# Optimization experiments

Hardware: AMD Instinct MI355X
Metric: run time of the kernel (lower is better)

The kernel has to match this reference:

```python
import jax, jax.numpy as jnp
import numpy as np

EMBED = 1024
HEADS = 16
HEAD_DIM = EMBED // HEADS
B, S = 4, 2048


def setup_inputs() -> dict:
    key = jax.random.key(0)
    ks = jax.random.split(key, 8)
    values = jax.random.normal(ks[0], (B, S, EMBED), dtype=jnp.float32)
    keys_in = jax.random.normal(ks[1], (B, S, EMBED), dtype=jnp.float32)
    query = jax.random.normal(ks[2], (B, S, EMBED), dtype=jnp.float32)
    mask = jnp.ones((B, 1, 1, S), dtype=jnp.int32)
    sc = 1.0 / np.sqrt(HEAD_DIM)
    Wv = jax.random.normal(ks[3], (HEAD_DIM, HEAD_DIM), dtype=jnp.float32) * sc
    Wk = jax.random.normal(ks[4], (HEAD_DIM, HEAD_DIM), dtype=jnp.float32) * sc
    Wq = jax.random.normal(ks[5], (HEAD_DIM, HEAD_DIM), dtype=jnp.float32) * sc
    Wo = jax.random.normal(ks[6], (EMBED, EMBED), dtype=jnp.float32) * (1.0 / np.sqrt(EMBED))
    bo = jnp.zeros((EMBED,), dtype=jnp.float32)
    return {"values": values, "keys": keys_in, "query": query, "mask": mask,
            "Wv": Wv, "Wk": Wk, "Wq": Wq, "Wo": Wo, "bo": bo}


def reference(values, keys, query, mask, Wv, Wk, Wq, Wo, bo):
    n = query.shape[0]
    vl, kl, ql = values.shape[1], keys.shape[1], query.shape[1]
    h, d = HEADS, HEAD_DIM
    # split heads: [n, len, h, d]
    v = values.reshape(n, vl, h, d)
    k = keys.reshape(n, kl, h, d)
    q = query.reshape(n, ql, h, d)
    # per-head linear projections (torch Linear: x @ W.T), shared across heads
    v = jnp.einsum('nlhd,ed->nlhe', v, Wv)
    k = jnp.einsum('nlhd,ed->nlhe', k, Wk)
    q = jnp.einsum('nlhd,ed->nlhe', q, Wq)
    # attention scores [n, h, q, k]
    energy = jnp.einsum('nqhd,nkhd->nhqk', q, k)
    energy = jnp.where(mask == 0, jnp.float32(-1e20), energy)
    # NOTE: original scales by sqrt(embed_size), not sqrt(head_dim)
    attn = jax.nn.softmax(energy / jnp.sqrt(jnp.float32(EMBED)), axis=3)
    out = jnp.einsum('nhql,nlhd->nqhd', attn, v).reshape(n, ql, h * d)
    return out @ Wo.T + bo
```

## Files before the change

### kernel.cpp

```cpp
#include <hip/hip_runtime.h>
#include <hip/hip_bf16.h>


#define SS 2048
#define HH 16
#define DD 64

typedef __attribute__((ext_vector_type(8))) short bf16x8;
typedef __attribute__((ext_vector_type(4))) short s16x4;
typedef __attribute__((ext_vector_type(4))) float f32x4;
typedef __attribute__((ext_vector_type(16))) float f32x16;

__device__ __forceinline__ short f2bf(float f) {
  union { float f; unsigned u; } c; c.f = f;
  unsigned r = (c.u + 0x7FFFu + ((c.u >> 16) & 1u)) >> 16;
  return (short)r;
}

__device__ __forceinline__ int cvtpk(float lo, float hi) {
  int r;
  asm("v_cvt_pk_bf16_f32 %0, %1, %2" : "=v"(r) : "v"(lo), "v"(hi));
  return r;
}

__device__ __forceinline__ float fexp2(float x) {
  float r;
  asm("v_exp_f32 %0, %1" : "=v"(r) : "v"(x));
  return r;
}

__global__ __launch_bounds__(256) void proj_kernel(
    const float* __restrict__ xq, const float* __restrict__ xk, const float* __restrict__ xv,
    const float* __restrict__ Wq, const float* __restrict__ Wk, const float* __restrict__ Wv,
    short* __restrict__ qp, short* __restrict__ kp, short* __restrict__ vp)
{
  __shared__ short xlds[128][72];
  __shared__ short wlds[3][64][72];
  const int t = threadIdx.x;
  const int lane = t & 63;
  const int w = t >> 6;
  const int l15 = lane & 15, l4 = lane >> 4;

  const float* wsrc[3] = {Wq, Wk, Wv};
#pragma unroll
  for (int z = 0; z < 3; ++z) {
#pragma unroll
    for (int i = 0; i < 4; ++i) {
      int fi = (t + i * 256) * 4;
      int row = fi >> 6, col = fi & 63;
      float4 a = *(const float4*)(wsrc[z] + fi);
      s16x4 sv = { f2bf(a.x), f2bf(a.y), f2bf(a.z), f2bf(a.w) };
      *(s16x4*)&wlds[z][row][col] = sv;
    }
  }

  const long r0 = (long)blockIdx.x * 128;
  const float* xin[3] = {xq, xk, xv};
  short* outp[3] = {qp, kp, vp};
  const float SCQ = 0.03125f * 1.4426950408889634f;

#pragma unroll
  for (int z = 0; z < 3; ++z) {
    __syncthreads();
    const float* src = xin[z] + r0 * 64;
#pragma unroll
    for (int i = 0; i < 8; ++i) {
      int fi = (t + i * 256) * 4;
      int row = fi >> 6, col = fi & 63;
      float4 a = *(const float4*)(src + fi);
      s16x4 sv = { f2bf(a.x), f2bf(a.y), f2bf(a.z), f2bf(a.w) };
      *(s16x4*)&xlds[row][col] = sv;
    }
    __syncthreads();

    bf16x8 af[2][2];
#pragma unroll
    for (int mi = 0; mi < 2; ++mi)
#pragma unroll
      for (int kb = 0; kb < 2; ++kb)
        af[mi][kb] = *(const bf16x8*)&xlds[w * 32 + mi * 16 + l15][kb * 32 + l4 * 8];

    f32x4 acc[2][4];
#pragma unroll
    for (int mi = 0; mi < 2; ++mi)
#pragma unroll
      for (int nt = 0; nt < 4; ++nt)
        acc[mi][nt] = (f32x4){0.f, 0.f, 0.f, 0.f};

#pragma unroll
    for (int nt = 0; nt < 4; ++nt)
#pragma unroll
      for (int kb = 0; kb < 2; ++kb) {
        bf16x8 bfr = *(const bf16x8*)&wlds[z][nt * 16 + l15][kb * 32 + l4 * 8];
#pragma unroll
        for (int mi = 0; mi < 2; ++mi)
          acc[mi][nt] = __builtin_amdgcn_mfma_f32_16x16x32_bf16(af[mi][kb], bfr, acc[mi][nt], 0, 0, 0);
      }

    short* dst = outp[z];
    const float sc = (z == 0) ? SCQ : 1.0f;
#pragma unroll
    for (int mi = 0; mi < 2; ++mi)
#pragma unroll
      for (int nt = 0; nt < 4; ++nt)
#pragma unroll
        for (int j = 0; j < 4; ++j) {
          int r = (int)r0 + w * 32 + mi * 16 + l4 * 4 + j;
          int e = nt * 16 + l15;
          int h = r & 15, bs = r >> 4;
          int b = bs >> 11, s = bs & 2047;
          dst[(((long)(b * 16 + h) * 2048 + s) << 6) + e] = f2bf(acc[mi][nt][j] * sc);
        }
  }
}

__global__ __launch_bounds__(256) void wo_cvt(const float* __restrict__ Wo,
                                              short* __restrict__ wob) {
  long i = ((long)blockIdx.x * 256 + threadIdx.x) * 4;
  float4 a = *(const float4*)(Wo + i);
  s16x4 sv = { f2bf(a.x), f2bf(a.y), f2bf(a.z), f2bf(a.w) };
  *(s16x4*)(wob + i) = sv;
}

__global__ __launch_bounds__(256) void vt_kernel(const short* __restrict__ vp,
                                                 short* __restrict__ vpt) {
  __shared__ short tl[64][72];
  const int t = threadIdx.x;
  const long base_in = (long)blockIdx.y * SS * DD + (long)blockIdx.x * 64 * DD;
#pragma unroll
  for (int i = 0; i < 2; ++i) {
    int c = t + i * 256;
    int s = c >> 3, d0 = (c & 7) * 8;
    bf16x8 v = *(const bf16x8*)(vp + base_in + s * 64 + d0);
#pragma unroll
    for (int j = 0; j < 8; ++j) tl[d0 + j][s] = v[j];
  }
  __syncthreads();
  const long base_out = (long)blockIdx.y * DD * SS + (long)blockIdx.x * 64;
#pragma unroll
  for (int i = 0; i < 2; ++i) {
    int c = t + i * 256;
    int d = c >> 3, s0 = (c & 7) * 8;
    *(bf16x8*)(vpt + base_out + (long)d * SS + s0) = *(const bf16x8*)&tl[d][s0];
  }
}

__global__ __launch_bounds__(256, 4) void attn_kernel(
    const short* __restrict__ qp, const short* __restrict__ kp, const short* __restrict__ vpt,
    const int* __restrict__ mask, short* __restrict__ ao)
{
  __shared__ short klds[2][64][72];
  __shared__ short vtlds[2][64][72];
  __shared__ int tile_ok[32];
  const int t = threadIdx.x, lane = t & 63, w = t >> 6;
  const int l31 = lane & 31, hi = lane >> 5;
  const int wg = (blockIdx.x & 7) * 128 + (blockIdx.x >> 3);
  const int bh = wg >> 4, qt = wg & 15;
  const int b = bh >> 4, h = bh & 15;
  const short* qb  = qp + (long)bh * SS * DD;
  const short* kbp = kp + (long)bh * SS * DD;
  const short* vtp = vpt + (long)bh * DD * SS;
  const int* mb = mask + b * SS;

  if (t < 32) tile_ok[t] = 1;
  __syncthreads();
  {
    int ok = 1;
#pragma unroll
    for (int i = 0; i < 8; ++i) ok &= (mb[t * 8 + i] != 0);
    if (!ok) tile_ok[t >> 3] = 0;
  }

  const int q = qt * 128 + w * 32 + l31;
  bf16x8 qf[4];
#pragma unroll
  for (int dblk = 0; dblk < 4; ++dblk)
    qf[dblk] = *(const bf16x8*)(qb + (long)q * 64 + dblk * 16 + hi * 8);

  const int sr = t >> 2;
  const int sc = (t & 3) * 16;
  const int v5 = sr & 31;
  const int prow = (sr & 32) + (v5 & 3) + 4 * ((v5 >> 3) & 1)
                 + 8 * (2 * ((v5 >> 4) & 1) + ((v5 >> 2) & 1));
  const short* kr_ptr = kbp + (long)sr * 64 + sc;
  const short* vr_ptr = vtp + (long)sr * SS + sc;

  bf16x8 kr0 = *(const bf16x8*)(kr_ptr);
  bf16x8 kr1 = *(const bf16x8*)(kr_ptr + 8);
  bf16x8 vr0 = *(const bf16x8*)(vr_ptr);
  bf16x8 vr1 = *(const bf16x8*)(vr_ptr + 8);
  *(bf16x8*)&klds[0][prow][sc]      = kr0;
  *(bf16x8*)&klds[0][prow][sc + 8]  = kr1;
  *(bf16x8*)&vtlds[0][sr][sc]       = vr0;
  *(bf16x8*)&vtlds[0][sr][sc + 8]   = vr1;
  kr0 = *(const bf16x8*)(kr_ptr + 64 * 64);
  kr1 = *(const bf16x8*)(kr_ptr + 64 * 64 + 8);
  vr0 = *(const bf16x8*)(vr_ptr + 64);
  vr1 = *(const bf16x8*)(vr_ptr + 64 + 8);

  const f32x16 fzero = {0.f,0.f,0.f,0.f,0.f,0.f,0.f,0.f,
                        0.f,0.f,0.f,0.f,0.f,0.f,0.f,0.f};
  f32x16 oacc[2];
  oacc[0] = fzero; oacc[1] = fzero;
  float l_reg = 0.f;

  for (int kt = 0; kt < SS / 64; ++kt) {
    const int cur = kt & 1, nxt = cur ^ 1;
    const int k0 = kt * 64;
    __syncthreads();
    *(bf16x8*)&klds[nxt][prow][sc]      = kr0;
    *(bf16x8*)&klds[nxt][prow][sc + 8]  = kr1;
    *(bf16x8*)&vtlds[nxt][sr][sc]       = vr0;
    *(bf16x8*)&vtlds[nxt][sr][sc + 8]   = vr1;

    f32x16 sacc[2];
    __builtin_amdgcn_s_setprio(1);
#pragma unroll
    for (int kb = 0; kb < 2; ++kb) {
      bf16x8 ka0 = *(const bf16x8*)&klds[cur][kb * 32 + l31][hi * 8];
      sacc[kb] = __builtin_amdgcn_mfma_f32_32x32x16_bf16(ka0, qf[0], fzero, 0, 0, 0);
#pragma unroll
      for (int dblk = 1; dblk < 4; ++dblk) {
        bf16x8 ka = *(const bf16x8*)&klds[cur][kb * 32 + l31][dblk * 16 + hi * 8];
        sacc[kb] = __builtin_amdgcn_mfma_f32_32x32x16_bf16(ka, qf[dblk], sacc[kb], 0, 0, 0);
      }
    }
    __builtin_amdgcn_s_setprio(0);

    if (!tile_ok[kt]) {
#pragma unroll
      for (int kb = 0; kb < 2; ++kb)
#pragma unroll
        for (int r = 0; r < 16; ++r) {
          int kv = k0 + kb * 32 + 16 * ((r >> 3) & 1) + 8 * hi
                 + 4 * ((r >> 2) & 1) + (r & 3);
          if (mb[kv] == 0) sacc[kb][r] = -1e30f;
        }
    }

    float s0 = 0.f, s1 = 0.f, s2 = 0.f, s3 = 0.f;
#pragma unroll
    for (int kb = 0; kb < 2; ++kb)
#pragma unroll
      for (int r = 0; r < 16; r += 4) {
        float p0 = fexp2(sacc[kb][r]);
        float p1 = fexp2(sacc[kb][r + 1]);
        float p2 = fexp2(sacc[kb][r + 2]);
        float p3 = fexp2(sacc[kb][r + 3]);
        sacc[kb][r] = p0; sacc[kb][r + 1] = p1;
        sacc[kb][r + 2] = p2; sacc[kb][r + 3] = p3;
        s0 += p0; s1 += p1; s2 += p2; s3 += p3;
      }
    float sum = (s0 + s1) + (s2 + s3);
    sum += __shfl_xor(sum, 32);
    l_reg += sum;

    union PW { int wd[4]; bf16x8 v; } pa[4];
#pragma unroll
    for (int kb = 0; kb < 2; ++kb)
#pragma unroll
      for (int s1i = 0; s1i < 2; ++s1i)
#pragma unroll
        for (int w2 = 0; w2 < 4; ++w2)
          pa[kb * 2 + s1i].wd[w2] =
              cvtpk(sacc[kb][8 * s1i + 2 * w2], sacc[kb][8 * s1i + 2 * w2 + 1]);

    __builtin_amdgcn_s_setprio(1);
#pragma unroll
    for (int dt = 0; dt < 2; ++dt)
#pragma unroll
      for (int ks = 0; ks < 4; ++ks) {
        bf16x8 va = *(const bf16x8*)&vtlds[cur][dt * 32 + l31][ks * 16 + hi * 8];
        oacc[dt] = __builtin_amdgcn_mfma_f32_32x32x16_bf16(va, pa[ks].v, oacc[dt], 0, 0, 0);
      }
    __builtin_amdgcn_s_setprio(0);

    {
      const int ktn = (kt < 30) ? kt + 2 : 31;
      const long k0n = (long)ktn * 64;
      kr0 = *(const bf16x8*)(kr_ptr + k0n * 64);
      kr1 = *(const bf16x8*)(kr_ptr + k0n * 64 + 8);
      vr0 = *(const bf16x8*)(vr_ptr + k0n);
      vr1 = *(const bf16x8*)(vr_ptr + k0n + 8);
    }
  }

  float inv = 1.f / l_reg;
#pragma unroll
  for (int dt = 0; dt < 2; ++dt)
#pragma unroll
    for (int g = 0; g < 4; ++g) {
      s16x4 sv;
#pragma unroll
      for (int j = 0; j < 4; ++j) sv[j] = f2bf(oacc[dt][g * 4 + j] * inv);
      int d0 = dt * 32 + g * 8 + hi * 4;
      *(s16x4*)(ao + (long)(b * SS + q) * 1024 + h * 64 + d0) = sv;
    }
}

__global__ __launch_bounds__(256) void out_gemm(
    const short* __restrict__ ao, const short* __restrict__ wob,
    const float* __restrict__ bo, float* __restrict__ out)
{
  __shared__ short alds[2][128][72];
  __shared__ short blds[2][128][72];
  const int t = threadIdx.x, lane = t & 63, w = t >> 6;
  const int l15 = lane & 15, l4 = lane >> 4;
  const int wm = w >> 1, wn = w & 1;
  const long m0 = (long)blockIdx.y * 128;
  const int n0 = blockIdx.x * 128;

  const int srow = t >> 3;
  const int scol = (t & 7) * 8;

  f32x4 acc[4][4];
#pragma unroll
  for (int mi = 0; mi < 4; ++mi)
#pragma unroll
    for (int ni = 0; ni < 4; ++ni) acc[mi][ni] = (f32x4){0.f, 0.f, 0.f, 0.f};

  bf16x8 ar[4], br[4];
#pragma unroll
  for (int i = 0; i < 4; ++i) {
    int row = srow + i * 32;
    ar[i] = *(const bf16x8*)(ao + (m0 + row) * 1024 + scol);
    br[i] = *(const bf16x8*)(wob + (long)(n0 + row) * 1024 + scol);
  }
#pragma unroll
  for (int i = 0; i < 4; ++i) {
    int row = srow + i * 32;
    *(bf16x8*)&alds[0][row][scol] = ar[i];
    *(bf16x8*)&blds[0][row][scol] = br[i];
  }
#pragma unroll
  for (int i = 0; i < 4; ++i) {
    int row = srow + i * 32;
    ar[i] = *(const bf16x8*)(ao + (m0 + row) * 1024 + 64 + scol);
    br[i] = *(const bf16x8*)(wob + (long)(n0 + row) * 1024 + 64 + scol);
  }

  for (int ki = 0; ki < 16; ++ki) {
    const int cur = ki & 1, nxt = cur ^ 1;
    __syncthreads();
#pragma unroll
    for (int i = 0; i < 4; ++i) {
      int row = srow + i * 32;
      *(bf16x8*)&alds[nxt][row][scol] = ar[i];
      *(bf16x8*)&blds[nxt][row][scol] = br[i];
    }
#pragma unroll
    for (int kb = 0; kb < 2; ++kb) {
      bf16x8 af[4], bfr[4];
#pragma unroll
      for (int mi = 0; mi < 4; ++mi)
        af[mi] = *(const bf16x8*)&alds[cur][wm * 64 + mi * 16 + l15][kb * 32 + l4 * 8];
#pragma unroll
      for (int ni = 0; ni < 4; ++ni)
        bfr[ni] = *(const bf16x8*)&blds[cur][wn * 64 + ni * 16 + l15][kb * 32 + l4 * 8];
#pragma unroll
      for (int mi = 0; mi < 4; ++mi)
#pragma unroll
        for (int ni = 0; ni < 4; ++ni)
          acc[mi][ni] = __builtin_amdgcn_mfma_f32_16x16x32_bf16(af[mi], bfr[ni], acc[mi][ni], 0, 0, 0);
    }
    {
      const int kn = ((ki < 14) ? ki + 2 : 15) * 64;
#pragma unroll
      for (int i = 0; i < 4; ++i) {
        int row = srow + i * 32;
        ar[i] = *(const bf16x8*)(ao + (m0 + row) * 1024 + kn + scol);
        br[i] = *(const bf16x8*)(wob + (long)(n0 + row) * 1024 + kn + scol);
      }
    }
  }
#pragma unroll
  for (int ni = 0; ni < 4; ++ni) {
    float bias = bo[n0 + wn * 64 + ni * 16 + l15];
#pragma unroll
    for (int mi = 0; mi < 4; ++mi)
#pragma unroll
      for (int j = 0; j < 4; ++j)
        out[(m0 + wm * 64 + mi * 16 + l4 * 4 + j) * 1024 + n0 + wn * 64 + ni * 16 + l15] =
            acc[mi][ni][j] + bias;
  }
}

extern "C" void kernel_launch(void* const* d_in, const int* in_sizes, int n_in,
                              void* d_out, int out_size, void* d_ws, size_t ws_size,
                              hipStream_t stream) {
  const float* values = (const float*)d_in[0];
  const float* keys   = (const float*)d_in[1];
  const float* query  = (const float*)d_in[2];
  const int*   mask   = (const int*)d_in[3];
  const float* Wv     = (const float*)d_in[4];
  const float* Wk     = (const float*)d_in[5];
  const float* Wq     = (const float*)d_in[6];
  const float* Wo     = (const float*)d_in[7];
  const float* bo     = (const float*)d_in[8];
  float* out = (float*)d_out;

  const long NTOK = 4L * SS * HH * DD;
  short* qp  = (short*)d_ws;
  short* kp  = qp + NTOK;
  short* vp  = kp + NTOK;
  short* aot = vp + NTOK;
  short* wob = aot + NTOK;
  short* vpt = wob + 1024 * 1024;

  hipLaunchKernelGGL(proj_kernel, dim3(1024), dim3(256), 0, stream,
                     query, keys, values, Wq, Wk, Wv, qp, kp, vp);
  hipLaunchKernelGGL(wo_cvt, dim3(1024), dim3(256), 0, stream, Wo, wob);
  hipLaunchKernelGGL(vt_kernel, dim3(32, 64), dim3(256), 0, stream, vp, vpt);
  hipLaunchKernelGGL(attn_kernel, dim3(1024), dim3(256), 0, stream,
                     qp, kp, vpt, mask, aot);
  hipLaunchKernelGGL(out_gemm, dim3(8, 64), dim3(256), 0, stream,
                     aot, wob, bo, out);
}
```

Baseline: 143.2 us.

## Software-pipeline attention loop with triple-buffered LDS and QK one tile ahead

Restructures the attention main loop so the QK^T MFMAs for tile t+1 are issued before the softmax and PV of tile t, and uses three LDS buffers for K and V instead of two. The aim is to overlap exp/convert VALU work with matrix-core work and to cut the barrier count to one per iteration. LDS row stride shrinks from 72 to 68 shorts, and occupancy is lowered from 4 to 3 blocks per CU to fit the extra buffer and the second score accumulator. Risks are higher register pressure, lower occupancy, and possible LDS bank conflicts from the new padding.

```diff
diff --git a/kernel.cpp b/kernel.cpp
--- a/kernel.cpp
+++ b/kernel.cpp
@@ -145,12 +145,107 @@
   }
 }
 
-__global__ __launch_bounds__(256, 4) void attn_kernel(
+#define LDW 68
+
+#define QK_PHASE(SNXT, PKB) do {                                               \
+  __builtin_amdgcn_s_setprio(1);                                               \
+  _Pragma("unroll")                                                            \
+  for (int kb_ = 0; kb_ < 2; ++kb_) {                                          \
+    const short* kp_ = (PKB) + (kb_ * 32 + l31) * LDW;                         \
+    bf16x8 ka0_ = *(const bf16x8*)(kp_ + hi * 8);                              \
+    SNXT[kb_] = __builtin_amdgcn_mfma_f32_32x32x16_bf16(ka0_, qf[0], fzero, 0, 0, 0); \
+    _Pragma("unroll")                                                          \
+    for (int db_ = 1; db_ < 4; ++db_) {                                        \
+      bf16x8 ka_ = *(const bf16x8*)(kp_ + db_ * 16 + hi * 8);                  \
+      SNXT[kb_] = __builtin_amdgcn_mfma_f32_32x32x16_bf16(ka_, qf[db_], SNXT[kb_], 0, 0, 0); \
+    }                                                                          \
+  }                                                                            \
+  __builtin_amdgcn_s_setprio(0);                                               \
+} while (0)
+
+#define STAGE_WR() do {                                                        \
+  *(bf16x8*)(pkC + koff_w)     = kr0;                                          \
+  *(bf16x8*)(pkC + koff_w + 8) = kr1;                                          \
+  *(bf16x8*)(pvC + voff_w)     = vr0;                                          \
+  *(bf16x8*)(pvC + voff_w + 8) = vr1;                                          \
+} while (0)
+
+#define PREFETCH(T3) do {                                                      \
+  const long o_ = (long)(T3);                                                  \
+  kr0 = *(const bf16x8*)(kr_ptr + o_ * 4096);                                  \
+  kr1 = *(const bf16x8*)(kr_ptr + o_ * 4096 + 8);                              \
+  vr0 = *(const bf16x8*)(vr_ptr + o_ * 64);                                    \
+  vr1 = *(const bf16x8*)(vr_ptr + o_ * 64 + 8);                                \
+} while (0)
+
+#define SM_PV(T, SCUR, PVA) do {                                               \
+  if (!tile_ok[(T)]) {                                                         \
+    const int k0_ = (T) * 64;                                                  \
+    _Pragma("unroll")                                                          \
+    for (int kb_ = 0; kb_ < 2; ++kb_)                                          \
+      _Pragma("unroll")                                                        \
+      for (int r_ = 0; r_ < 16; ++r_) {                                        \
+        int kv_ = k0_ + kb_ * 32 + 16 * ((r_ >> 3) & 1) + 8 * hi               \
+                + 4 * ((r_ >> 2) & 1) + (r_ & 3);                              \
+        if (mb[kv_] == 0) SCUR[kb_][r_] = -1e30f;                              \
+      }                                                                        \
+  }                                                                            \
+  float s0_ = 0.f, s1_ = 0.f, s2_ = 0.f, s3_ = 0.f;                            \
+  _Pragma("unroll")                                                            \
+  for (int kb_ = 0; kb_ < 2; ++kb_)                                            \
+    _Pragma("unroll")                                                          \
+    for (int r_ = 0; r_ < 16; r_ += 4) {                                       \
+      float p0_ = fexp2(SCUR[kb_][r_]);                                        \
+      float p1_ = fexp2(SCUR[kb_][r_ + 1]);                                    \
+      float p2_ = fexp2(SCUR[kb_][r_ + 2]);                                    \
+      float p3_ = fexp2(SCUR[kb_][r_ + 3]);                                    \
+      SCUR[kb_][r_] = p0_; SCUR[kb_][r_ + 1] = p1_;                            \
+      SCUR[kb_][r_ + 2] = p2_; SCUR[kb_][r_ + 3] = p3_;                        \
+      s0_ += p0_; s1_ += p1_; s2_ += p2_; s3_ += p3_;                          \
+    }                                                                          \
+  float sum_ = (s0_ + s1_) + (s2_ + s3_);                                      \
+  sum_ += __shfl_xor(sum_, 32);                                                \
+  l_reg += sum_;                                                               \
+  union PW { int wd[4]; bf16x8 v; } pa_[4];                                    \
+  _Pragma("unroll")                                                            \
+  for (int kb_ = 0; kb_ < 2; ++kb_)                                            \
+    _Pragma("unroll")                                                          \
+    for (int s1i_ = 0; s1i_ < 2; ++s1i_)                                       \
+      _Pragma("unroll")                                                        \
+      for (int w2_ = 0; w2_ < 4; ++w2_)                                        \
+        pa_[kb_ * 2 + s1i_].wd[w2_] =                                          \
+            cvtpk(SCUR[kb_][8 * s1i_ + 2 * w2_], SCUR[kb_][8 * s1i_ + 2 * w2_ + 1]); \
+  __builtin_amdgcn_s_setprio(1);                                               \
+  _Pragma("unroll")                                                            \
+  for (int dt_ = 0; dt_ < 2; ++dt_)                                            \
+    _Pragma("unroll")                                                          \
+    for (int ks_ = 0; ks_ < 4; ++ks_) {                                        \
+      bf16x8 va_ = *(const bf16x8*)((PVA) + (dt_ * 32 + l31) * LDW + ks_ * 16 + hi * 8); \
+      oacc[dt_] = __builtin_amdgcn_mfma_f32_32x32x16_bf16(va_, pa_[ks_].v, oacc[dt_], 0, 0, 0); \
+    }                                                                          \
+  __builtin_amdgcn_s_setprio(0);                                               \
+} while (0)
+
+#define ROT() do {                                                             \
+  short* tp_ = pkA; pkA = pkB; pkB = pkC; pkC = tp_;                           \
+  tp_ = pvA; pvA = pvB; pvB = pvC; pvC = tp_;                                  \
+} while (0)
+
+#define ITER(T, SCUR, SNXT) do {                                               \
+  QK_PHASE(SNXT, pkB);                                                         \
+  STAGE_WR();                                                                  \
+  SM_PV((T), SCUR, pvA);                                                       \
+  PREFETCH(((T) + 3 < 31) ? (T) + 3 : 31);                                     \
+  __syncthreads();                                                             \
+  ROT();                                                                       \
+} while (0)
+
+__global__ __launch_bounds__(256, 3) void attn_kernel(
     const short* __restrict__ qp, const short* __restrict__ kp, const short* __restrict__ vpt,
     const int* __restrict__ mask, short* __restrict__ ao)
 {
-  __shared__ short klds[2][64][72];
-  __shared__ short vtlds[2][64][72];
+  __shared__ short kbuf[3][64][LDW];
+  __shared__ short vbuf[3][64][LDW];
   __shared__ int tile_ok[32];
   const int t = threadIdx.x, lane = t & 63, w = t >> 6;
   const int l31 = lane & 31, hi = lane >> 5;
@@ -182,108 +277,39 @@
   const int v5 = sr & 31;
   const int prow = (sr & 32) + (v5 & 3) + 4 * ((v5 >> 3) & 1)
                  + 8 * (2 * ((v5 >> 4) & 1) + ((v5 >> 2) & 1));
+  const int koff_w = prow * LDW + sc;
+  const int voff_w = sr * LDW + sc;
   const short* kr_ptr = kbp + (long)sr * 64 + sc;
   const short* vr_ptr = vtp + (long)sr * SS + sc;
 
-  bf16x8 kr0 = *(const bf16x8*)(kr_ptr);
-  bf16x8 kr1 = *(const bf16x8*)(kr_ptr + 8);
-  bf16x8 vr0 = *(const bf16x8*)(vr_ptr);
-  bf16x8 vr1 = *(const bf16x8*)(vr_ptr + 8);
-  *(bf16x8*)&klds[0][prow][sc]      = kr0;
-  *(bf16x8*)&klds[0][prow][sc + 8]  = kr1;
-  *(bf16x8*)&vtlds[0][sr][sc]       = vr0;
-  *(bf16x8*)&vtlds[0][sr][sc + 8]   = vr1;
-  kr0 = *(const bf16x8*)(kr_ptr + 64 * 64);
-  kr1 = *(const bf16x8*)(kr_ptr + 64 * 64 + 8);
-  vr0 = *(const bf16x8*)(vr_ptr + 64);
-  vr1 = *(const bf16x8*)(vr_ptr + 64 + 8);
+  short* pkA = &kbuf[0][0][0]; short* pkB = &kbuf[1][0][0]; short* pkC = &kbuf[2][0][0];
+  short* pvA = &vbuf[0][0][0]; short* pvB = &vbuf[1][0][0]; short* pvC = &vbuf[2][0][0];
 
   const f32x16 fzero = {0.f,0.f,0.f,0.f,0.f,0.f,0.f,0.f,
                         0.f,0.f,0.f,0.f,0.f,0.f,0.f,0.f};
   f32x16 oacc[2];
   oacc[0] = fzero; oacc[1] = fzero;
   float l_reg = 0.f;
-
-  for (int kt = 0; kt < SS / 64; ++kt) {
-    const int cur = kt & 1, nxt = cur ^ 1;
-    const int k0 = kt * 64;
-    __syncthreads();
-    *(bf16x8*)&klds[nxt][prow][sc]      = kr0;
-    *(bf16x8*)&klds[nxt][prow][sc + 8]  = kr1;
-    *(bf16x8*)&vtlds[nxt][sr][sc]       = vr0;
-    *(bf16x8*)&vtlds[nxt][sr][sc + 8]   = vr1;
-
-    f32x16 sacc[2];
-    __builtin_amdgcn_s_setprio(1);
-#pragma unroll
-    for (int kb = 0; kb < 2; ++kb) {
-      bf16x8 ka0 = *(const bf16x8*)&klds[cur][kb * 32 + l31][hi * 8];
-      sacc[kb] = __builtin_amdgcn_mfma_f32_32x32x16_bf16(ka0, qf[0], fzero, 0, 0, 0);
-#pragma unroll
-      for (int dblk = 1; dblk < 4; ++dblk) {
-        bf16x8 ka = *(const bf16x8*)&klds[cur][kb * 32 + l31][dblk * 16 + hi * 8];
-        sacc[kb] = __builtin_amdgcn_mfma_f32_32x32x16_bf16(ka, qf[dblk], sacc[kb], 0, 0, 0);
-      }
-    }
-    __builtin_amdgcn_s_setprio(0);
-
-    if (!tile_ok[kt]) {
-#pragma unroll
-      for (int kb = 0; kb < 2; ++kb)
-#pragma unroll
-        for (int r = 0; r < 16; ++r) {
-          int kv = k0 + kb * 32 + 16 * ((r >> 3) & 1) + 8 * hi
-                 + 4 * ((r >> 2) & 1) + (r & 3);
-          if (mb[kv] == 0) sacc[kb][r] = -1e30f;
-        }
-    }
-
-    float s0 = 0.f, s1 = 0.f, s2 = 0.f, s3 = 0.f;
-#pragma unroll
-    for (int kb = 0; kb < 2; ++kb)
-#pragma unroll
-      for (int r = 0; r < 16; r += 4) {
-        float p0 = fexp2(sacc[kb][r]);
-        float p1 = fexp2(sacc[kb][r + 1]);
-        float p2 = fexp2(sacc[kb][r + 2]);
-        float p3 = fexp2(sacc[kb][r + 3]);
-        sacc[kb][r] = p0; sacc[kb][r + 1] = p1;
-        sacc[kb][r + 2] = p2; sacc[kb][r + 3] = p3;
-        s0 += p0; s1 += p1; s2 += p2; s3 += p3;
-      }
-    float sum = (s0 + s1) + (s2 + s3);
-    sum += __shfl_xor(sum, 32);
-    l_reg += sum;
-
-    union PW { int wd[4]; bf16x8 v; } pa[4];
-#pragma unroll
-    for (int kb = 0; kb < 2; ++kb)
-#pragma unroll
-      for (int s1i = 0; s1i < 2; ++s1i)
-#pragma unroll
-        for (int w2 = 0; w2 < 4; ++w2)
-          pa[kb * 2 + s1i].wd[w2] =
-              cvtpk(sacc[kb][8 * s1i + 2 * w2], sacc[kb][8 * s1i + 2 * w2 + 1]);
-
-    __builtin_amdgcn_s_setprio(1);
-#pragma unroll
-    for (int dt = 0; dt < 2; ++dt)
-#pragma unroll
-      for (int ks = 0; ks < 4; ++ks) {
-        bf16x8 va = *(const bf16x8*)&vtlds[cur][dt * 32 + l31][ks * 16 + hi * 8];
-        oacc[dt] = __builtin_amdgcn_mfma_f32_32x32x16_bf16(va, pa[ks].v, oacc[dt], 0, 0, 0);
-      }
-    __builtin_amdgcn_s_setprio(0);
-
-    {
-      const int ktn = (kt < 30) ? kt + 2 : 31;
-      const long k0n = (long)ktn * 64;
-      kr0 = *(const bf16x8*)(kr_ptr + k0n * 64);
-      kr1 = *(const bf16x8*)(kr_ptr + k0n * 64 + 8);
-      vr0 = *(const bf16x8*)(vr_ptr + k0n);
-      vr1 = *(const bf16x8*)(vr_ptr + k0n + 8);
-    }
-  }
+  bf16x8 kr0, kr1, vr0, vr1;
+
+  PREFETCH(0);
+  *(bf16x8*)(pkA + koff_w) = kr0; *(bf16x8*)(pkA + koff_w + 8) = kr1;
+  *(bf16x8*)(pvA + voff_w) = vr0; *(bf16x8*)(pvA + voff_w + 8) = vr1;
+  PREFETCH(1);
+  *(bf16x8*)(pkB + koff_w) = kr0; *(bf16x8*)(pkB + koff_w + 8) = kr1;
+  *(bf16x8*)(pvB + voff_w) = vr0; *(bf16x8*)(pvB + voff_w + 8) = vr1;
+  PREFETCH(2);
+  __syncthreads();
+
+  f32x16 sA[2], sB[2];
+  QK_PHASE(sA, pkA);
+
+  for (int kt = 0; kt < 30; kt += 2) {
+    ITER(kt, sA, sB);
+    ITER(kt + 1, sB, sA);
+  }
+  ITER(30, sA, sB);
+  SM_PV(31, sB, pvA);
 
   float inv = 1.f / l_reg;
 #pragma unroll
```

Result: slower. 392.0 us (+173.8%).

## Restructure attention to 8 waves using 16x16x32 MFMA tiles

Applied to the files above, without the earlier changes.

The attention kernel moves from 4 waves with 32x32x16 MFMAs (32 queries per wave) to 8 waves with 16x16x32 MFMAs (16 queries per wave), doubling the block to 512 threads. The goal is smaller per-wave accumulators, lower register pressure and more waves to hide LDS and global latency. Each thread now loads one bf16x8 chunk of K and V per tile instead of two, the LDS row padding shrinks from 72 to 68, and the next-tile prefetch is issued earlier, right after the QK MFMAs. The 68-short row stride leaves the 16-byte LDS vector accesses without 16-byte alignment, which may split or serialise them, and the tighter launch bounds may cause spills.

```diff
diff --git a/kernel.cpp b/kernel.cpp
--- a/kernel.cpp
+++ b/kernel.cpp
@@ -9,7 +9,6 @@
 typedef __attribute__((ext_vector_type(8))) short bf16x8;
 typedef __attribute__((ext_vector_type(4))) short s16x4;
 typedef __attribute__((ext_vector_type(4))) float f32x4;
-typedef __attribute__((ext_vector_type(16))) float f32x16;
 
 __device__ __forceinline__ short f2bf(float f) {
   union { float f; unsigned u; } c; c.f = f;
@@ -145,15 +144,15 @@
   }
 }
 
-__global__ __launch_bounds__(256, 4) void attn_kernel(
+__global__ __launch_bounds__(512, 8) void attn_kernel(
     const short* __restrict__ qp, const short* __restrict__ kp, const short* __restrict__ vpt,
     const int* __restrict__ mask, short* __restrict__ ao)
 {
-  __shared__ short klds[2][64][72];
-  __shared__ short vtlds[2][64][72];
+  __shared__ short klds[2][64][68];
+  __shared__ short vtlds[2][64][68];
   __shared__ int tile_ok[32];
   const int t = threadIdx.x, lane = t & 63, w = t >> 6;
-  const int l31 = lane & 31, hi = lane >> 5;
+  const int l15 = lane & 15, l4 = (lane >> 4) & 3;
   const int wg = (blockIdx.x & 7) * 128 + (blockIdx.x >> 3);
   const int bh = wg >> 4, qt = wg & 15;
   const int b = bh >> 4, h = bh & 15;
@@ -167,135 +166,110 @@
   {
     int ok = 1;
 #pragma unroll
-    for (int i = 0; i < 8; ++i) ok &= (mb[t * 8 + i] != 0);
-    if (!ok) tile_ok[t >> 3] = 0;
-  }
-
-  const int q = qt * 128 + w * 32 + l31;
-  bf16x8 qf[4];
-#pragma unroll
-  for (int dblk = 0; dblk < 4; ++dblk)
-    qf[dblk] = *(const bf16x8*)(qb + (long)q * 64 + dblk * 16 + hi * 8);
-
-  const int sr = t >> 2;
-  const int sc = (t & 3) * 16;
-  const int v5 = sr & 31;
-  const int prow = (sr & 32) + (v5 & 3) + 4 * ((v5 >> 3) & 1)
-                 + 8 * (2 * ((v5 >> 4) & 1) + ((v5 >> 2) & 1));
-  const short* kr_ptr = kbp + (long)sr * 64 + sc;
-  const short* vr_ptr = vtp + (long)sr * SS + sc;
-
-  bf16x8 kr0 = *(const bf16x8*)(kr_ptr);
-  bf16x8 kr1 = *(const bf16x8*)(kr_ptr + 8);
-  bf16x8 vr0 = *(const bf16x8*)(vr_ptr);
-  bf16x8 vr1 = *(const bf16x8*)(vr_ptr + 8);
-  *(bf16x8*)&klds[0][prow][sc]      = kr0;
-  *(bf16x8*)&klds[0][prow][sc + 8]  = kr1;
-  *(bf16x8*)&vtlds[0][sr][sc]       = vr0;
-  *(bf16x8*)&vtlds[0][sr][sc + 8]   = vr1;
-  kr0 = *(const bf16x8*)(kr_ptr + 64 * 64);
-  kr1 = *(const bf16x8*)(kr_ptr + 64 * 64 + 8);
-  vr0 = *(const bf16x8*)(vr_ptr + 64);
-  vr1 = *(const bf16x8*)(vr_ptr + 64 + 8);
-
-  const f32x16 fzero = {0.f,0.f,0.f,0.f,0.f,0.f,0.f,0.f,
-                        0.f,0.f,0.f,0.f,0.f,0.f,0.f,0.f};
-  f32x16 oacc[2];
-  oacc[0] = fzero; oacc[1] = fzero;
+    for (int i = 0; i < 4; ++i) ok &= (mb[t * 4 + i] != 0);
+    if (!ok) tile_ok[t >> 4] = 0;
+  }
+
+  const int q = qt * 128 + w * 16 + l15;
+  bf16x8 qf0 = *(const bf16x8*)(qb + (long)q * 64 + l4 * 8);
+  bf16x8 qf1 = *(const bf16x8*)(qb + (long)q * 64 + 32 + l4 * 8);
+
+  const int skv = t >> 3;
+  const int ssc = (t & 7) * 8;
+  const int prow = 32 * (skv >> 5) + 16 * ((skv >> 2) & 1)
+                 + 4 * ((skv >> 3) & 3) + (skv & 3);
+  const short* kr_ptr = kbp + (long)skv * 64 + ssc;
+  const short* vr_ptr = vtp + (long)skv * SS + ssc;
+
+  bf16x8 kr = *(const bf16x8*)kr_ptr;
+  bf16x8 vr = *(const bf16x8*)vr_ptr;
+  *(bf16x8*)&klds[0][prow][ssc]  = kr;
+  *(bf16x8*)&vtlds[0][skv][ssc]  = vr;
+  kr = *(const bf16x8*)(kr_ptr + 4096);
+  vr = *(const bf16x8*)(vr_ptr + 64);
+
+  const f32x4 fz4 = {0.f, 0.f, 0.f, 0.f};
+  f32x4 oacc[4];
+#pragma unroll
+  for (int dblk = 0; dblk < 4; ++dblk) oacc[dblk] = fz4;
   float l_reg = 0.f;
 
-  for (int kt = 0; kt < SS / 64; ++kt) {
+  for (int kt = 0; kt < 32; ++kt) {
     const int cur = kt & 1, nxt = cur ^ 1;
-    const int k0 = kt * 64;
     __syncthreads();
-    *(bf16x8*)&klds[nxt][prow][sc]      = kr0;
-    *(bf16x8*)&klds[nxt][prow][sc + 8]  = kr1;
-    *(bf16x8*)&vtlds[nxt][sr][sc]       = vr0;
-    *(bf16x8*)&vtlds[nxt][sr][sc + 8]   = vr1;
-
-    f32x16 sacc[2];
+    *(bf16x8*)&klds[nxt][prow][ssc] = kr;
+    *(bf16x8*)&vtlds[nxt][skv][ssc] = vr;
+
+    f32x4 sacc[4];
     __builtin_amdgcn_s_setprio(1);
 #pragma unroll
-    for (int kb = 0; kb < 2; ++kb) {
-      bf16x8 ka0 = *(const bf16x8*)&klds[cur][kb * 32 + l31][hi * 8];
-      sacc[kb] = __builtin_amdgcn_mfma_f32_32x32x16_bf16(ka0, qf[0], fzero, 0, 0, 0);
-#pragma unroll
-      for (int dblk = 1; dblk < 4; ++dblk) {
-        bf16x8 ka = *(const bf16x8*)&klds[cur][kb * 32 + l31][dblk * 16 + hi * 8];
-        sacc[kb] = __builtin_amdgcn_mfma_f32_32x32x16_bf16(ka, qf[dblk], sacc[kb], 0, 0, 0);
-      }
+    for (int k4 = 0; k4 < 4; ++k4) {
+      bf16x8 ka0 = *(const bf16x8*)&klds[cur][k4 * 16 + l15][l4 * 8];
+      sacc[k4] = __builtin_amdgcn_mfma_f32_16x16x32_bf16(ka0, qf0, fz4, 0, 0, 0);
+      bf16x8 ka1 = *(const bf16x8*)&klds[cur][k4 * 16 + l15][32 + l4 * 8];
+      sacc[k4] = __builtin_amdgcn_mfma_f32_16x16x32_bf16(ka1, qf1, sacc[k4], 0, 0, 0);
     }
     __builtin_amdgcn_s_setprio(0);
 
+    {
+      const int ktn = (kt < 30) ? kt + 2 : 31;
+      kr = *(const bf16x8*)(kr_ptr + (long)ktn * 4096);
+      vr = *(const bf16x8*)(vr_ptr + (long)ktn * 64);
+    }
+
     if (!tile_ok[kt]) {
 #pragma unroll
-      for (int kb = 0; kb < 2; ++kb)
-#pragma unroll
-        for (int r = 0; r < 16; ++r) {
-          int kv = k0 + kb * 32 + 16 * ((r >> 3) & 1) + 8 * hi
-                 + 4 * ((r >> 2) & 1) + (r & 3);
-          if (mb[kv] == 0) sacc[kb][r] = -1e30f;
+      for (int k4 = 0; k4 < 4; ++k4)
+#pragma unroll
+        for (int r = 0; r < 4; ++r) {
+          int kv = kt * 64 + 32 * (k4 >> 1) + 8 * l4 + 4 * (k4 & 1) + r;
+          if (mb[kv] == 0) sacc[k4][r] = -1e30f;
         }
     }
 
     float s0 = 0.f, s1 = 0.f, s2 = 0.f, s3 = 0.f;
 #pragma unroll
-    for (int kb = 0; kb < 2; ++kb)
-#pragma unroll
-      for (int r = 0; r < 16; r += 4) {
-        float p0 = fexp2(sacc[kb][r]);
-        float p1 = fexp2(sacc[kb][r + 1]);
-        float p2 = fexp2(sacc[kb][r + 2]);
-        float p3 = fexp2(sacc[kb][r + 3]);
-        sacc[kb][r] = p0; sacc[kb][r + 1] = p1;
-        sacc[kb][r + 2] = p2; sacc[kb][r + 3] = p3;
-        s0 += p0; s1 += p1; s2 += p2; s3 += p3;
-      }
+    for (int k4 = 0; k4 < 4; ++k4) {
+      float p0 = fexp2(sacc[k4][0]);
+      float p1 = fexp2(sacc[k4][1]);
+      float p2 = fexp2(sacc[k4][2]);
+      float p3 = fexp2(sacc[k4][3]);
+      sacc[k4][0] = p0; sacc[k4][1] = p1; sacc[k4][2] = p2; sacc[k4][3] = p3;
+      s0 += p0; s1 += p1; s2 += p2; s3 += p3;
+    }
     float sum = (s0 + s1) + (s2 + s3);
+    sum += __shfl_xor(sum, 16);
     sum += __shfl_xor(sum, 32);
     l_reg += sum;
 
-    union PW { int wd[4]; bf16x8 v; } pa[4];
-#pragma unroll
-    for (int kb = 0; kb < 2; ++kb)
-#pragma unroll
-      for (int s1i = 0; s1i < 2; ++s1i)
-#pragma unroll
-        for (int w2 = 0; w2 < 4; ++w2)
-          pa[kb * 2 + s1i].wd[w2] =
-              cvtpk(sacc[kb][8 * s1i + 2 * w2], sacc[kb][8 * s1i + 2 * w2 + 1]);
+    union PW { int wd[4]; bf16x8 v; } pa[2];
+#pragma unroll
+    for (int b2 = 0; b2 < 2; ++b2) {
+      pa[b2].wd[0] = cvtpk(sacc[2 * b2][0], sacc[2 * b2][1]);
+      pa[b2].wd[1] = cvtpk(sacc[2 * b2][2], sacc[2 * b2][3]);
+      pa[b2].wd[2] = cvtpk(sacc[2 * b2 + 1][0], sacc[2 * b2 + 1][1]);
+      pa[b2].wd[3] = cvtpk(sacc[2 * b2 + 1][2], sacc[2 * b2 + 1][3]);
+    }
 
     __builtin_amdgcn_s_setprio(1);
 #pragma unroll
-    for (int dt = 0; dt < 2; ++dt)
-#pragma unroll
-      for (int ks = 0; ks < 4; ++ks) {
-        bf16x8 va = *(const bf16x8*)&vtlds[cur][dt * 32 + l31][ks * 16 + hi * 8];
-        oacc[dt] = __builtin_amdgcn_mfma_f32_32x32x16_bf16(va, pa[ks].v, oacc[dt], 0, 0, 0);
+    for (int dblk = 0; dblk < 4; ++dblk)
+#pragma unroll
+      for (int b2 = 0; b2 < 2; ++b2) {
+        bf16x8 va = *(const bf16x8*)&vtlds[cur][dblk * 16 + l15][b2 * 32 + l4 * 8];
+        oacc[dblk] = __builtin_amdgcn_mfma_f32_16x16x32_bf16(va, pa[b2].v, oacc[dblk], 0, 0, 0);
       }
     __builtin_amdgcn_s_setprio(0);
-
-    {
-      const int ktn = (kt < 30) ? kt + 2 : 31;
-      const long k0n = (long)ktn * 64;
-      kr0 = *(const bf16x8*)(kr_ptr + k0n * 64);
-      kr1 = *(const bf16x8*)(kr_ptr + k0n * 64 + 8);
-      vr0 = *(const bf16x8*)(vr_ptr + k0n);
-      vr1 = *(const bf16x8*)(vr_ptr + k0n + 8);
-    }
   }
 
   float inv = 1.f / l_reg;
 #pragma unroll
-  for (int dt = 0; dt < 2; ++dt)
-#pragma unroll
-    for (int g = 0; g < 4; ++g) {
-      s16x4 sv;
-#pragma unroll
-      for (int j = 0; j < 4; ++j) sv[j] = f2bf(oacc[dt][g * 4 + j] * inv);
-      int d0 = dt * 32 + g * 8 + hi * 4;
-      *(s16x4*)(ao + (long)(b * SS + q) * 1024 + h * 64 + d0) = sv;
-    }
+  for (int dblk = 0; dblk < 4; ++dblk) {
+    s16x4 sv;
+#pragma unroll
+    for (int j = 0; j < 4; ++j) sv[j] = f2bf(oacc[dblk][j] * inv);
+    *(s16x4*)(ao + (long)(b * SS + q) * 1024 + h * 64 + dblk * 16 + l4 * 4) = sv;
+  }
 }
 
 __global__ __launch_bounds__(256) void out_gemm(
@@ -411,7 +385,7 @@
                      query, keys, values, Wq, Wk, Wv, qp, kp, vp);
   hipLaunchKernelGGL(wo_cvt, dim3(1024), dim3(256), 0, stream, Wo, wob);
   hipLaunchKernelGGL(vt_kernel, dim3(32, 64), dim3(256), 0, stream, vp, vpt);
-  hipLaunchKernelGGL(attn_kernel, dim3(1024), dim3(256), 0, stream,
+  hipLaunchKernelGGL(attn_kernel, dim3(1024), dim3(512), 0, stream,
                      qp, kp, vpt, mask, aot);
   hipLaunchKernelGGL(out_gemm, dim3(8, 64), dim3(256), 0, stream,
                      aot, wob, bo, out);
```

Measured after the change: 175.8 us. 1.23x slower.

## Process two 32-row query fragments per wave in attention kernel

Applied to the files above, without the earlier changes.

Each wave now handles 64 query rows (two 32-row MFMA fragments) instead of 32, so each block covers 256 queries and the grid halves to 512 blocks. Every K/V fragment loaded from LDS is reused for two MFMAs, halving LDS reads and global K/V traffic per query. The prefetch of the next tile is moved ahead of the softmax, and the LDS row padding shrinks from 72 to 68. The cost is roughly double the accumulator registers, occupancy lowered to 2 blocks per CU, and fewer blocks to spread over the CUs.

```diff
diff --git a/kernel.cpp b/kernel.cpp
--- a/kernel.cpp
+++ b/kernel.cpp
@@ -145,17 +145,17 @@
   }
 }
 
-__global__ __launch_bounds__(256, 4) void attn_kernel(
+__global__ __launch_bounds__(256, 2) void attn_kernel(
     const short* __restrict__ qp, const short* __restrict__ kp, const short* __restrict__ vpt,
     const int* __restrict__ mask, short* __restrict__ ao)
 {
-  __shared__ short klds[2][64][72];
-  __shared__ short vtlds[2][64][72];
+  __shared__ short klds[2][64][68];
+  __shared__ short vtlds[2][64][68];
   __shared__ int tile_ok[32];
   const int t = threadIdx.x, lane = t & 63, w = t >> 6;
   const int l31 = lane & 31, hi = lane >> 5;
-  const int wg = (blockIdx.x & 7) * 128 + (blockIdx.x >> 3);
-  const int bh = wg >> 4, qt = wg & 15;
+  const int wg = (blockIdx.x & 7) * 64 + (blockIdx.x >> 3);
+  const int bh = wg >> 3, qt = wg & 7;
   const int b = bh >> 4, h = bh & 15;
   const short* qb  = qp + (long)bh * SS * DD;
   const short* kbp = kp + (long)bh * SS * DD;
@@ -171,11 +171,13 @@
     if (!ok) tile_ok[t >> 3] = 0;
   }
 
-  const int q = qt * 128 + w * 32 + l31;
-  bf16x8 qf[4];
-#pragma unroll
-  for (int dblk = 0; dblk < 4; ++dblk)
-    qf[dblk] = *(const bf16x8*)(qb + (long)q * 64 + dblk * 16 + hi * 8);
+  const int q0 = qt * 256 + w * 64;
+  bf16x8 qf[2][4];
+#pragma unroll
+  for (int f = 0; f < 2; ++f)
+#pragma unroll
+    for (int dblk = 0; dblk < 4; ++dblk)
+      qf[f][dblk] = *(const bf16x8*)(qb + (long)(q0 + f * 32 + l31) * 64 + dblk * 16 + hi * 8);
 
   const int sr = t >> 2;
   const int sc = (t & 3) * 16;
@@ -193,16 +195,17 @@
   *(bf16x8*)&klds[0][prow][sc + 8]  = kr1;
   *(bf16x8*)&vtlds[0][sr][sc]       = vr0;
   *(bf16x8*)&vtlds[0][sr][sc + 8]   = vr1;
-  kr0 = *(const bf16x8*)(kr_ptr + 64 * 64);
-  kr1 = *(const bf16x8*)(kr_ptr + 64 * 64 + 8);
+  kr0 = *(const bf16x8*)(kr_ptr + 4096);
+  kr1 = *(const bf16x8*)(kr_ptr + 4096 + 8);
   vr0 = *(const bf16x8*)(vr_ptr + 64);
   vr1 = *(const bf16x8*)(vr_ptr + 64 + 8);
 
   const f32x16 fzero = {0.f,0.f,0.f,0.f,0.f,0.f,0.f,0.f,
                         0.f,0.f,0.f,0.f,0.f,0.f,0.f,0.f};
-  f32x16 oacc[2];
-  oacc[0] = fzero; oacc[1] = fzero;
-  float l_reg = 0.f;
+  f32x16 oacc[2][2];
+#pragma unroll
+  for (int f = 0; f < 2; ++f) { oacc[f][0] = fzero; oacc[f][1] = fzero; }
+  float l_acc[2] = {0.f, 0.f};
 
   for (int kt = 0; kt < SS / 64; ++kt) {
     const int cur = kt & 1, nxt = cur ^ 1;
@@ -213,66 +216,20 @@
     *(bf16x8*)&vtlds[nxt][sr][sc]       = vr0;
     *(bf16x8*)&vtlds[nxt][sr][sc + 8]   = vr1;
 
-    f32x16 sacc[2];
+    f32x16 sacc[2][2];
     __builtin_amdgcn_s_setprio(1);
 #pragma unroll
     for (int kb = 0; kb < 2; ++kb) {
       bf16x8 ka0 = *(const bf16x8*)&klds[cur][kb * 32 + l31][hi * 8];
-      sacc[kb] = __builtin_amdgcn_mfma_f32_32x32x16_bf16(ka0, qf[0], fzero, 0, 0, 0);
+      sacc[0][kb] = __builtin_amdgcn_mfma_f32_32x32x16_bf16(ka0, qf[0][0], fzero, 0, 0, 0);
+      sacc[1][kb] = __builtin_amdgcn_mfma_f32_32x32x16_bf16(ka0, qf[1][0], fzero, 0, 0, 0);
 #pragma unroll
       for (int dblk = 1; dblk < 4; ++dblk) {
         bf16x8 ka = *(const bf16x8*)&klds[cur][kb * 32 + l31][dblk * 16 + hi * 8];
-        sacc[kb] = __builtin_amdgcn_mfma_f32_32x32x16_bf16(ka, qf[dblk], sacc[kb], 0, 0, 0);
-      }
-    }
-    __builtin_amdgcn_s_setprio(0);
-
-    if (!tile_ok[kt]) {
-#pragma unroll
-      for (int kb = 0; kb < 2; ++kb)
-#pragma unroll
-        for (int r = 0; r < 16; ++r) {
-          int kv = k0 + kb * 32 + 16 * ((r >> 3) & 1) + 8 * hi
-                 + 4 * ((r >> 2) & 1) + (r & 3);
-          if (mb[kv] == 0) sacc[kb][r] = -1e30f;
-        }
-    }
-
-    float s0 = 0.f, s1 = 0.f, s2 = 0.f, s3 = 0.f;
-#pragma unroll
-    for (int kb = 0; kb < 2; ++kb)
-#pragma unroll
-      for (int r = 0; r < 16; r += 4) {
-        float p0 = fexp2(sacc[kb][r]);
-        float p1 = fexp2(sacc[kb][r + 1]);
-        float p2 = fexp2(sacc[kb][r + 2]);
-        float p3 = fexp2(sacc[kb][r + 3]);
-        sacc[kb][r] = p0; sacc[kb][r + 1] = p1;
-        sacc[kb][r + 2] = p2; sacc[kb][r + 3] = p3;
-        s0 += p0; s1 += p1; s2 += p2; s3 += p3;
-      }
-    float sum = (s0 + s1) + (s2 + s3);
-    sum += __shfl_xor(sum, 32);
-    l_reg += sum;
-
-    union PW { int wd[4]; bf16x8 v; } pa[4];
-#pragma unroll
-    for (int kb = 0; kb < 2; ++kb)
-#pragma unroll
-      for (int s1i = 0; s1i < 2; ++s1i)
-#pragma unroll
-        for (int w2 = 0; w2 < 4; ++w2)
-          pa[kb * 2 + s1i].wd[w2] =
-              cvtpk(sacc[kb][8 * s1i + 2 * w2], sacc[kb][8 * s1i + 2 * w2 + 1]);
-
-    __builtin_amdgcn_s_setprio(1);
-#pragma unroll
-    for (int dt = 0; dt < 2; ++dt)
-#pragma unroll
-      for (int ks = 0; ks < 4; ++ks) {
-        bf16x8 va = *(const bf16x8*)&vtlds[cur][dt * 32 + l31][ks * 16 + hi * 8];
-        oacc[dt] = __builtin_amdgcn_mfma_f32_32x32x16_bf16(va, pa[ks].v, oacc[dt], 0, 0, 0);
-      }
+        sacc[0][kb] = __builtin_amdgcn_mfma_f32_32x32x16_bf16(ka, qf[0][dblk], sacc[0][kb], 0, 0, 0);
+        sacc[1][kb] = __builtin_amdgcn_mfma_f32_32x32x16_bf16(ka, qf[1][dblk], sacc[1][kb], 0, 0, 0);
+      }
+    }
     __builtin_amdgcn_s_setprio(0);
 
     {
@@ -283,19 +240,73 @@
       vr0 = *(const bf16x8*)(vr_ptr + k0n);
       vr1 = *(const bf16x8*)(vr_ptr + k0n + 8);
     }
-  }
-
-  float inv = 1.f / l_reg;
-#pragma unroll
-  for (int dt = 0; dt < 2; ++dt)
-#pragma unroll
-    for (int g = 0; g < 4; ++g) {
-      s16x4 sv;
-#pragma unroll
-      for (int j = 0; j < 4; ++j) sv[j] = f2bf(oacc[dt][g * 4 + j] * inv);
-      int d0 = dt * 32 + g * 8 + hi * 4;
-      *(s16x4*)(ao + (long)(b * SS + q) * 1024 + h * 64 + d0) = sv;
-    }
+
+    union PW { int wd[4]; bf16x8 v; } pa[2][4];
+#pragma unroll
+    for (int f = 0; f < 2; ++f) {
+      if (!tile_ok[kt]) {
+#pragma unroll
+        for (int kb = 0; kb < 2; ++kb)
+#pragma unroll
+          for (int r = 0; r < 16; ++r) {
+            int kv = k0 + kb * 32 + 16 * ((r >> 3) & 1) + 8 * hi
+                   + 4 * ((r >> 2) & 1) + (r & 3);
+            if (mb[kv] == 0) sacc[f][kb][r] = -1e30f;
+          }
+      }
+      float s0 = 0.f, s1 = 0.f, s2 = 0.f, s3 = 0.f;
+#pragma unroll
+      for (int kb = 0; kb < 2; ++kb)
+#pragma unroll
+        for (int r = 0; r < 16; r += 4) {
+          float p0 = fexp2(sacc[f][kb][r]);
+          float p1 = fexp2(sacc[f][kb][r + 1]);
+          float p2 = fexp2(sacc[f][kb][r + 2]);
+          float p3 = fexp2(sacc[f][kb][r + 3]);
+          sacc[f][kb][r] = p0; sacc[f][kb][r + 1] = p1;
+          sacc[f][kb][r + 2] = p2; sacc[f][kb][r + 3] = p3;
+          s0 += p0; s1 += p1; s2 += p2; s3 += p3;
+        }
+      float sum = (s0 + s1) + (s2 + s3);
+      sum += __shfl_xor(sum, 32);
+      l_acc[f] += sum;
+#pragma unroll
+      for (int kb = 0; kb < 2; ++kb)
+#pragma unroll
+        for (int s1i = 0; s1i < 2; ++s1i)
+#pragma unroll
+          for (int w2 = 0; w2 < 4; ++w2)
+            pa[f][kb * 2 + s1i].wd[w2] =
+                cvtpk(sacc[f][kb][8 * s1i + 2 * w2], sacc[f][kb][8 * s1i + 2 * w2 + 1]);
+    }
+
+    __builtin_amdgcn_s_setprio(1);
+#pragma unroll
+    for (int dt = 0; dt < 2; ++dt)
+#pragma unroll
+      for (int ks = 0; ks < 4; ++ks) {
+        bf16x8 va = *(const bf16x8*)&vtlds[cur][dt * 32 + l31][ks * 16 + hi * 8];
+        oacc[0][dt] = __builtin_amdgcn_mfma_f32_32x32x16_bf16(va, pa[0][ks].v, oacc[0][dt], 0, 0, 0);
+        oacc[1][dt] = __builtin_amdgcn_mfma_f32_32x32x16_bf16(va, pa[1][ks].v, oacc[1][dt], 0, 0, 0);
+      }
+    __builtin_amdgcn_s_setprio(0);
+  }
+
+#pragma unroll
+  for (int f = 0; f < 2; ++f) {
+    float inv = 1.f / l_acc[f];
+    const int q = q0 + f * 32 + l31;
+#pragma unroll
+    for (int dt = 0; dt < 2; ++dt)
+#pragma unroll
+      for (int g = 0; g < 4; ++g) {
+        s16x4 sv;
+#pragma unroll
+        for (int j = 0; j < 4; ++j) sv[j] = f2bf(oacc[f][dt][g * 4 + j] * inv);
+        int d0 = dt * 32 + g * 8 + hi * 4;
+        *(s16x4*)(ao + (long)(b * SS + q) * 1024 + h * 64 + d0) = sv;
+      }
+  }
 }
 
 __global__ __launch_bounds__(256) void out_gemm(
@@ -411,7 +422,7 @@
                      query, keys, values, Wq, Wk, Wv, qp, kp, vp);
   hipLaunchKernelGGL(wo_cvt, dim3(1024), dim3(256), 0, stream, Wo, wob);
   hipLaunchKernelGGL(vt_kernel, dim3(32, 64), dim3(256), 0, stream, vp, vpt);
-  hipLaunchKernelGGL(attn_kernel, dim3(1024), dim3(256), 0, stream,
+  hipLaunchKernelGGL(attn_kernel, dim3(512), dim3(256), 0, stream,
                      qp, kp, vpt, mask, aot);
   hipLaunchKernelGGL(out_gemm, dim3(8, 64), dim3(256), 0, stream,
                      aot, wob, bo, out);
```

Result: faster. 139.5 us (-2.5%).
